# Optimization experiments

Hardware: AMD Instinct MI355X
Metric: run time of the kernel (lower is better)

## Reference

```python
import jax, jax.numpy as jnp
import numpy as np

B, S, HID = 2, 2048, 2048
H, KV, D = 16, 4, 128
EPS = 1e-6
ROPE_THETA = 1000000.0


def _rope_tables():
    inv_freq = 1.0 / (ROPE_THETA ** (jnp.arange(0, D, 2, dtype=jnp.float32) / D))  # [D/2]
    pos = jnp.arange(S, dtype=jnp.float32)
    freqs = pos[:, None] * inv_freq[None, :]            # [S, D/2]
    emb = jnp.concatenate([freqs, freqs], axis=-1)      # [S, D]
    cos = jnp.broadcast_to(jnp.cos(emb)[None], (B, S, D))
    sin = jnp.broadcast_to(jnp.sin(emb)[None], (B, S, D))
    return cos, sin


def setup_inputs() -> dict:
    key = jax.random.key(0)
    ks = jax.random.split(key, 6)
    cos, sin = _rope_tables()
    return {
        "hidden_states": jax.random.normal(ks[0], (B, S, HID), dtype=jnp.float32),
        "cos": cos,
        "sin": sin,
        "Wq": jax.random.normal(ks[1], (2 * H * D, HID), dtype=jnp.float32) * 0.02,
        "Wk": jax.random.normal(ks[2], (KV * D, HID), dtype=jnp.float32) * 0.02,
        "Wv": jax.random.normal(ks[3], (KV * D, HID), dtype=jnp.float32) * 0.02,
        "Wo": jax.random.normal(ks[4], (HID, H * D), dtype=jnp.float32) * 0.02,
        "q_norm_w": jnp.zeros((D,), dtype=jnp.float32),
        "k_norm_w": jnp.zeros((D,), dtype=jnp.float32),
    }


def _rms_norm(x, w):
    # (1+weight) parameterization, computed in fp32 as in the torch module
    xf = x.astype(jnp.float32)
    inv = jax.lax.rsqrt(jnp.mean(xf * xf, axis=-1, keepdims=True) + EPS)
    return (xf * inv * (1.0 + w.astype(jnp.float32))).astype(x.dtype)


def _rotate_half(x):
    h = x.shape[-1] // 2
    return jnp.concatenate([-x[..., h:], x[..., :h]], axis=-1)


def reference(hidden_states, cos, sin, Wq, Wk, Wv, Wo, q_norm_w, k_norm_w):
    b, s, _ = hidden_states.shape
    # Q projection yields interleaved (query, gate) per head: [B,S,H,2D]
    qg = jnp.einsum('bsh,oh->bso', hidden_states, Wq).reshape(b, s, H, 2 * D)
    q = qg[..., :D]                                   # [B,S,H,D]
    gate = qg[..., D:].reshape(b, s, H * D)           # [B,S,H*D]

    q = _rms_norm(q, q_norm_w).transpose(0, 2, 1, 3)                              # [B,H,S,D]
    k = _rms_norm(jnp.einsum('bsh,oh->bso', hidden_states, Wk).reshape(b, s, KV, D),
                  k_norm_w).transpose(0, 2, 1, 3)                                 # [B,KV,S,D]
    v = jnp.einsum('bsh,oh->bso', hidden_states, Wv).reshape(b, s, KV, D).transpose(0, 2, 1, 3)

    # RoPE (HF convention: cos/sin [B,S,D] broadcast over heads)
    c = cos[:, None, :, :]
    si = sin[:, None, :, :]
    q = q * c + _rotate_half(q) * si
    k = k * c + _rotate_half(k) * si

    # GQA repeat_kv: each kv head repeated n_rep times contiguously
    n_rep = H // KV
    k = jnp.repeat(k, n_rep, axis=1)   # [B,H,S,D]
    v = jnp.repeat(v, n_rep, axis=1)

    scale = D ** -0.5
    scores = jnp.einsum('bhqd,bhkd->bhqk', q, k) * scale                         # [B,H,S,S]
    causal = jnp.tril(jnp.ones((s, s), dtype=bool))
    scores = jnp.where(causal[None, None], scores, jnp.finfo(scores.dtype).min)
    probs = jax.nn.softmax(scores, axis=-1)
    attn = jnp.einsum('bhqk,bhkd->bhqd', probs, v)                               # [B,H,S,D]

    attn = attn.transpose(0, 2, 1, 3).reshape(b, s, H * D)
    attn = attn * jax.nn.sigmoid(gate)
    return jnp.einsum('bsh,oh->bso', attn, Wo)
```

## Files before the change

### kernel.cpp

```cpp
#include <hip/hip_runtime.h>
#include <stdint.h>


using bf16 = unsigned short;
typedef __attribute__((ext_vector_type(8)))  short bf16x8;
typedef __attribute__((ext_vector_type(4)))  float f32x4;
typedef __attribute__((ext_vector_type(16))) float f32x16;

__device__ __forceinline__ unsigned short f2bf(float x) {
  unsigned int u = __float_as_uint(x);
  unsigned int r = u + 0x7fffu + ((u >> 16) & 1u);
  return (unsigned short)(r >> 16);
}

__device__ __forceinline__ unsigned int pk2(float a, float b) {
  return (unsigned int)f2bf(a) | ((unsigned int)f2bf(b) << 16);
}

__device__ __forceinline__ void async_copy16(const void* g, void* l) {
  __builtin_amdgcn_global_load_lds(
      (const __attribute__((address_space(1))) void*)g,
      (__attribute__((address_space(3))) void*)l, 16, 0, 0);
}

__global__ void f2b_kernel(const float* __restrict__ in, bf16* __restrict__ out) {
  int i = (blockIdx.x * 256 + threadIdx.x) * 4;
  float4 v = *(const float4*)(in + i);
  ushort4 o;
  o.x = f2bf(v.x); o.y = f2bf(v.y); o.z = f2bf(v.z); o.w = f2bf(v.w);
  *(ushort4*)(out + i) = o;
}

__global__ __launch_bounds__(256) void gemm_bt(const bf16* __restrict__ A,
                                               const bf16* __restrict__ B,
                                               float* __restrict__ C,
                                               int M, int N, int K) {
  __shared__ __align__(16) bf16 As[128 * 32];
  __shared__ __align__(16) bf16 Bs[128 * 32];
  const int tid = threadIdx.x;
  const int w = tid >> 6, lane = tid & 63;
  const int wr = w >> 1, wc = w & 1;
  const int li = lane & 15, hi = lane >> 4;

  const int nbx = gridDim.x, nwg = nbx * gridDim.y;
  const int orig = blockIdx.y * nbx + blockIdx.x;
  const int tileid = (orig & 7) * (nwg >> 3) + (orig >> 3);
  const int bm = (tileid / nbx) * 128, bn = (tileid % nbx) * 128;

  f32x4 acc[4][4];
#pragma unroll
  for (int m = 0; m < 4; m++)
#pragma unroll
    for (int n = 0; n < 4; n++) acc[m][n] = (f32x4){0.f, 0.f, 0.f, 0.f};

  const int c0 = tid, c1 = tid + 256;
  const bf16* Ab = A + (long long)bm * K;
  const bf16* Bb = B + (long long)bn * K;

  for (int k0 = 0; k0 < K; k0 += 32) {
    async_copy16(Ab + (c0 >> 2) * K + k0 + (c0 & 3) * 8, (char*)As + c0 * 16);
    async_copy16(Ab + (c1 >> 2) * K + k0 + (c1 & 3) * 8, (char*)As + c1 * 16);
    async_copy16(Bb + (c0 >> 2) * K + k0 + (c0 & 3) * 8, (char*)Bs + c0 * 16);
    async_copy16(Bb + (c1 >> 2) * K + k0 + (c1 & 3) * 8, (char*)Bs + c1 * 16);
    __syncthreads();

    bf16x8 af[4], bfv[4];
#pragma unroll
    for (int m = 0; m < 4; m++)
      af[m] = *(const bf16x8*)(As + (wr * 64 + m * 16 + li) * 32 + hi * 8);
#pragma unroll
    for (int n = 0; n < 4; n++)
      bfv[n] = *(const bf16x8*)(Bs + (wc * 64 + n * 16 + li) * 32 + hi * 8);
#pragma unroll
    for (int m = 0; m < 4; m++)
#pragma unroll
      for (int n = 0; n < 4; n++)
        acc[m][n] = __builtin_amdgcn_mfma_f32_16x16x32_bf16(af[m], bfv[n],
                                                            acc[m][n], 0, 0, 0);
    __syncthreads();
  }

#pragma unroll
  for (int m = 0; m < 4; m++)
#pragma unroll
    for (int n = 0; n < 4; n++) {
      int row = bm + wr * 64 + m * 16 + hi * 4;
      int col = bn + wc * 64 + n * 16 + li;
#pragma unroll
      for (int r = 0; r < 4; r++) C[(long long)(row + r) * N + col] = acc[m][n][r];
    }
}

__global__ __launch_bounds__(256) void pack_qk(
    const float* __restrict__ qg_raw, const float* __restrict__ kv_raw,
    const float* __restrict__ cosb, const float* __restrict__ sinb,
    const float* __restrict__ qnw, const float* __restrict__ knw,
    bf16* __restrict__ q_pack, bf16* __restrict__ k_pack) {
  int rowid = blockIdx.x * 4 + (threadIdx.x >> 6);
  int lane = threadIdx.x & 63;
  int token = rowid / 20, r = rowid % 20;
  int b = token >> 11, s = token & 2047;
  const float* src; const float* wn; bf16* dst; float scale;
  if (r < 16) {
    src = qg_raw + (long long)token * 4096 + r * 256;
    wn = qnw;
    dst = q_pack + ((long long)(b * 16 + r) * 2048 + s) * 128;
    scale = 0.08838834764831845f;
  } else {
    int kv = r - 16;
    src = kv_raw + (long long)token * 1024 + kv * 128;
    wn = knw;
    dst = k_pack + ((long long)(b * 4 + kv) * 2048 + s) * 128;
    scale = 1.0f;
  }
  float x0 = src[lane], x1 = src[lane + 64];
  float ss = x0 * x0 + x1 * x1;
#pragma unroll
  for (int off = 32; off > 0; off >>= 1) ss += __shfl_xor(ss, off);
  float inv = rsqrtf(ss * (1.0f / 128.0f) + 1e-6f);
  float n0 = x0 * inv * (1.f + wn[lane]);
  float n1 = x1 * inv * (1.f + wn[lane + 64]);
  const float* cp = cosb + (long long)(b * 2048 + s) * 128;
  const float* sp = sinb + (long long)(b * 2048 + s) * 128;
  dst[lane]      = f2bf((n0 * cp[lane]      - n1 * sp[lane])      * scale);
  dst[lane + 64] = f2bf((n1 * cp[lane + 64] + n0 * sp[lane + 64]) * scale);
}

__global__ __launch_bounds__(256) void transpose_v(const float* __restrict__ kv_raw,
                                                   bf16* __restrict__ vt) {
  __shared__ float tile[32][33];
  int b = blockIdx.z;
  int c0 = blockIdx.x * 32;
  int s0 = blockIdx.y * 32;
  int tx = threadIdx.x & 31, ty = threadIdx.x >> 5;
#pragma unroll
  for (int i = 0; i < 32; i += 8)
    tile[ty + i][tx] = kv_raw[(long long)(b * 2048 + s0 + ty + i) * 1024 + 512 + c0 + tx];
  __syncthreads();
#pragma unroll
  for (int i = 0; i < 32; i += 8)
    vt[(long long)(b * 512 + c0 + ty + i) * 2048 + s0 + tx] = f2bf(tile[tx][ty + i]);
}

__global__ __launch_bounds__(256) void attn_kernel(
    const bf16* __restrict__ qp, const bf16* __restrict__ kp,
    const bf16* __restrict__ vt, const float* __restrict__ qg_raw,
    bf16* __restrict__ attn_g) {
  const int w = threadIdx.x >> 6, lane = threadIdx.x & 63;
  const int l31 = lane & 31, hi2 = lane >> 5;
  const int bh = blockIdx.y, b = bh >> 4, h = bh & 15, kv = h >> 2;
  const int qtile = (gridDim.x - 1) - blockIdx.x;
  const int q0w = qtile * 128 + w * 32;
  const int q = q0w + l31;

  const bf16* qb = qp + ((long long)(b * 16 + h) * 2048 + q0w) * 128;
  const bf16* kb = kp + (long long)(b * 4 + kv) * 2048 * 128;
  const bf16* vb = vt + (long long)(b * 4 + kv) * 128 * 2048;

  bf16x8 qf[8];
#pragma unroll
  for (int d = 0; d < 8; d++)
    qf[d] = *(const bf16x8*)(qb + l31 * 128 + d * 16 + hi2 * 8);

  f32x16 O[4];
#pragma unroll
  for (int ct = 0; ct < 4; ct++)
#pragma unroll
    for (int i = 0; i < 16; i++) O[ct][i] = 0.f;

  float mval = -1e30f, lsum = 0.f;
  const int ktmax = q0w >> 5;

  bf16x8 kf[8];
#pragma unroll
  for (int d = 0; d < 8; d++)
    kf[d] = *(const bf16x8*)(kb + l31 * 128 + d * 16 + hi2 * 8);

  for (int kt = 0; kt <= ktmax; kt++) {
    const int k0 = kt * 32;

    f32x16 s;
#pragma unroll
    for (int i = 0; i < 16; i++) s[i] = 0.f;
#pragma unroll
    for (int d = 0; d < 8; d++)
      s = __builtin_amdgcn_mfma_f32_32x32x16_bf16(kf[d], qf[d], s, 0, 0, 0);

    const int k0n = (kt < ktmax) ? (k0 + 32) : k0;
#pragma unroll
    for (int d = 0; d < 8; d++)
      kf[d] = *(const bf16x8*)(kb + (k0n + l31) * 128 + d * 16 + hi2 * 8);

    bf16x8 vf[8];
#pragma unroll
    for (int ct = 0; ct < 4; ct++)
#pragma unroll
      for (int kc = 0; kc < 2; kc++)
        vf[ct * 2 + kc] =
            *(const bf16x8*)(vb + (ct * 32 + l31) * 2048 + k0 + kc * 16 + hi2 * 8);

    if (k0 + 31 > q0w) {
#pragma unroll
      for (int r = 0; r < 16; r++) {
        int kk = k0 + (r & 3) + 8 * (r >> 2) + 4 * hi2;
        if (kk > q) s[r] = -1e30f;
      }
    }

    float pm = s[0];
#pragma unroll
    for (int r = 1; r < 16; r++) pm = fmaxf(pm, s[r]);
    pm = fmaxf(pm, __shfl_xor(pm, 32));

    int keep = __all(pm <= mval + 8.0f);
    float mn = mval, alpha = 1.f;
    if (!keep) {
      mn = fmaxf(mval, pm);
      alpha = __expf(mval - mn);
      mval = mn;
    }
    float sum = 0.f;
#pragma unroll
    for (int r = 0; r < 16; r++) { s[r] = __expf(s[r] - mn); sum += s[r]; }
    sum += __shfl_xor(sum, 32);
    if (keep) {
      lsum += sum;
    } else {
      lsum = lsum * alpha + sum;
#pragma unroll
      for (int ct = 0; ct < 4; ct++)
#pragma unroll
        for (int i = 0; i < 16; i++) O[ct][i] *= alpha;
    }

    bf16x8 pf[2];
#pragma unroll
    for (int kc = 0; kc < 2; kc++) {
      unsigned int wA = pk2(s[8 * kc + 0], s[8 * kc + 1]);
      unsigned int wB = pk2(s[8 * kc + 2], s[8 * kc + 3]);
      unsigned int wC = pk2(s[8 * kc + 4], s[8 * kc + 5]);
      unsigned int wD = pk2(s[8 * kc + 6], s[8 * kc + 7]);
      unsigned int xA = (unsigned int)__shfl_xor((int)wA, 32);
      unsigned int xB = (unsigned int)__shfl_xor((int)wB, 32);
      unsigned int xC = (unsigned int)__shfl_xor((int)wC, 32);
      unsigned int xD = (unsigned int)__shfl_xor((int)wD, 32);
      union { unsigned int u[4]; bf16x8 v; } pu;
      pu.u[0] = hi2 ? xC : wA;
      pu.u[1] = hi2 ? xD : wB;
      pu.u[2] = hi2 ? wC : xA;
      pu.u[3] = hi2 ? wD : xB;
      pf[kc] = pu.v;
    }

#pragma unroll
    for (int ct = 0; ct < 4; ct++) {
      O[ct] = __builtin_amdgcn_mfma_f32_32x32x16_bf16(vf[ct * 2 + 0], pf[0], O[ct], 0, 0, 0);
      O[ct] = __builtin_amdgcn_mfma_f32_32x32x16_bf16(vf[ct * 2 + 1], pf[1], O[ct], 0, 0, 0);
    }
  }

  const float linv = 1.f / lsum;
  const long long tok = (long long)(b * 2048 + q);
#pragma unroll
  for (int ct = 0; ct < 4; ct++)
#pragma unroll
    for (int r = 0; r < 16; r++) {
      int c = ct * 32 + (r & 3) + 8 * (r >> 2) + 4 * hi2;
      float g = qg_raw[tok * 4096 + h * 256 + 128 + c];
      float val = O[ct][r] * linv * (1.f / (1.f + __expf(-g)));
      attn_g[tok * 2048 + h * 128 + c] = f2bf(val);
    }
}

extern "C" void kernel_launch(void* const* d_in, const int* in_sizes, int n_in,
                              void* d_out, int out_size, void* d_ws, size_t ws_size,
                              hipStream_t stream) {
  const float* hs   = (const float*)d_in[0];
  const float* cosb = (const float*)d_in[1];
  const float* sinb = (const float*)d_in[2];
  const float* Wq   = (const float*)d_in[3];
  const float* Wk   = (const float*)d_in[4];
  const float* Wv   = (const float*)d_in[5];
  const float* Wo   = (const float*)d_in[6];
  const float* qnw  = (const float*)d_in[7];
  const float* knw  = (const float*)d_in[8];
  float* out = (float*)d_out;

  const size_t WS_NEEDED = 130023424ull;
  if (ws_size < WS_NEEDED) return;

  char* p = (char*)d_ws;
  bf16*  hs_bf  = (bf16*)p;  p += 4096ull * 2048 * 2;
  bf16*  wq_bf  = (bf16*)p;  p += 4096ull * 2048 * 2;
  bf16*  wkv_bf = (bf16*)p;  p += 1024ull * 2048 * 2;
  bf16*  wo_bf  = (bf16*)p;  p += 2048ull * 2048 * 2;
  float* qg_raw = (float*)p; p += 4096ull * 4096 * 4;
  float* kv_raw = (float*)p; p += 4096ull * 1024 * 4;
  bf16* q_pack = (bf16*)hs_bf;
  bf16* k_pack = (bf16*)wq_bf;
  bf16* vt     = (bf16*)((char*)wq_bf + 2ull * 4 * 2048 * 128 * 2);
  bf16* attn_g = (bf16*)kv_raw;

  f2b_kernel<<<8192, 256, 0, stream>>>(hs, hs_bf);
  f2b_kernel<<<8192, 256, 0, stream>>>(Wq, wq_bf);
  f2b_kernel<<<1024, 256, 0, stream>>>(Wk, wkv_bf);
  f2b_kernel<<<1024, 256, 0, stream>>>(Wv, wkv_bf + 512 * 2048);
  f2b_kernel<<<4096, 256, 0, stream>>>(Wo, wo_bf);

  gemm_bt<<<dim3(32, 32), 256, 0, stream>>>(hs_bf, wq_bf, qg_raw, 4096, 4096, 2048);
  gemm_bt<<<dim3(8, 32), 256, 0, stream>>>(hs_bf, wkv_bf, kv_raw, 4096, 1024, 2048);

  pack_qk<<<20480, 256, 0, stream>>>(qg_raw, kv_raw, cosb, sinb, qnw, knw, q_pack, k_pack);
  transpose_v<<<dim3(16, 64, 2), 256, 0, stream>>>(kv_raw, vt);

  attn_kernel<<<dim3(16, 32), 256, 0, stream>>>(q_pack, k_pack, vt, qg_raw, attn_g);

  gemm_bt<<<dim3(16, 32), 256, 0, stream>>>(attn_g, wo_bf, out, 4096, 2048, 2048);
}
```

Measured before the change: 612.4 us.

## Stage K/V tiles in LDS with double-buffered async copies shared across waves

The attention kernel now loads each 32-key K tile and V tile once per block into swizzled LDS buffers using async global-to-LDS copies. It double-buffers them so the next tile is fetched while the current one is computed, and all four waves share the tile instead of each reading it from global memory. The V transpose kernel writes a tile-blocked layout so each key tile is one contiguous 8 KB chunk. The cost is a block-wide barrier every iteration and a block-uniform loop bound, so lower waves run extra fully masked tiles.

Result: faster. 557.4 us (-9.0%).

```diff
diff --git a/kernel.cpp b/kernel.cpp
--- a/kernel.cpp
+++ b/kernel.cpp
@@ -137,15 +137,21 @@
   for (int i = 0; i < 32; i += 8)
     tile[ty + i][tx] = kv_raw[(long long)(b * 2048 + s0 + ty + i) * 1024 + 512 + c0 + tx];
   __syncthreads();
-#pragma unroll
-  for (int i = 0; i < 32; i += 8)
-    vt[(long long)(b * 512 + c0 + ty + i) * 2048 + s0 + tx] = f2bf(tile[tx][ty + i]);
+  int kt = s0 >> 5;
+#pragma unroll
+  for (int i = 0; i < 32; i += 8) {
+    int cg = c0 + ty + i;
+    int kvh = cg >> 7, c = cg & 127;
+    vt[((long long)(b * 4 + kvh) * 64 + kt) * 4096 + c * 32 + tx] = f2bf(tile[tx][ty + i]);
+  }
 }
 
 __global__ __launch_bounds__(256) void attn_kernel(
     const bf16* __restrict__ qp, const bf16* __restrict__ kp,
     const bf16* __restrict__ vt, const float* __restrict__ qg_raw,
     bf16* __restrict__ attn_g) {
+  __shared__ __align__(16) char Ks[2][8192];
+  __shared__ __align__(16) char Vs[2][8192];
   const int w = threadIdx.x >> 6, lane = threadIdx.x & 63;
   const int l31 = lane & 31, hi2 = lane >> 5;
   const int bh = blockIdx.y, b = bh >> 4, h = bh & 15, kv = h >> 2;
@@ -154,8 +160,19 @@
   const int q = q0w + l31;
 
   const bf16* qb = qp + ((long long)(b * 16 + h) * 2048 + q0w) * 128;
-  const bf16* kb = kp + (long long)(b * 4 + kv) * 2048 * 128;
-  const bf16* vb = vt + (long long)(b * 4 + kv) * 128 * 2048;
+  const char* kbb = (const char*)(kp + (long long)(b * 4 + kv) * 2048 * 128);
+  const char* vbb = (const char*)(vt + (long long)(b * 4 + kv) * 64 * 4096);
+
+  int ksrco[2], vsrco[2], dsto[2];
+#pragma unroll
+  for (int i = 0; i < 2; i++) {
+    int p = (w * 2 + i) * 64 + lane;
+    int rk = p >> 4, gk = p & 15;
+    ksrco[i] = rk * 256 + ((gk ^ (rk & 15)) << 4);
+    int rv = p >> 2, gv = p & 3;
+    vsrco[i] = rv * 64 + ((gv ^ ((rv >> 1) & 3)) << 4);
+    dsto[i] = p << 4;
+  }
 
   bf16x8 qf[8];
 #pragma unroll
@@ -169,15 +186,40 @@
     for (int i = 0; i < 16; i++) O[ct][i] = 0.f;
 
   float mval = -1e30f, lsum = 0.f;
-  const int ktmax = q0w >> 5;
-
-  bf16x8 kf[8];
-#pragma unroll
-  for (int d = 0; d < 8; d++)
-    kf[d] = *(const bf16x8*)(kb + l31 * 128 + d * 16 + hi2 * 8);
-
-  for (int kt = 0; kt <= ktmax; kt++) {
+  const int ktmaxb = qtile * 4 + 3;
+
+#pragma unroll
+  for (int i = 0; i < 2; i++) {
+    async_copy16(kbb + ksrco[i], &Ks[0][dsto[i]]);
+    async_copy16(vbb + vsrco[i], &Vs[0][dsto[i]]);
+  }
+  __syncthreads();
+
+  for (int kt = 0; kt <= ktmaxb; kt++) {
+    const int bi = kt & 1;
     const int k0 = kt * 32;
+
+    if (kt < ktmaxb) {
+      const char* ksrc = kbb + (long long)(kt + 1) * 8192;
+      const char* vsrc = vbb + (long long)(kt + 1) * 8192;
+#pragma unroll
+      for (int i = 0; i < 2; i++) {
+        async_copy16(ksrc + ksrco[i], &Ks[bi ^ 1][dsto[i]]);
+        async_copy16(vsrc + vsrco[i], &Vs[bi ^ 1][dsto[i]]);
+      }
+    }
+
+    bf16x8 kf[8];
+#pragma unroll
+    for (int d = 0; d < 8; d++)
+      kf[d] = *(const bf16x8*)&Ks[bi][l31 * 256 + (((d * 2 + hi2) ^ (l31 & 15)) << 4)];
+    bf16x8 vf[8];
+#pragma unroll
+    for (int ct = 0; ct < 4; ct++)
+#pragma unroll
+      for (int kc = 0; kc < 2; kc++)
+        vf[ct * 2 + kc] = *(const bf16x8*)
+            &Vs[bi][(ct * 32 + l31) * 64 + (((kc * 2 + hi2) ^ ((l31 >> 1) & 3)) << 4)];
 
     f32x16 s;
 #pragma unroll
@@ -185,19 +227,6 @@
 #pragma unroll
     for (int d = 0; d < 8; d++)
       s = __builtin_amdgcn_mfma_f32_32x32x16_bf16(kf[d], qf[d], s, 0, 0, 0);
-
-    const int k0n = (kt < ktmax) ? (k0 + 32) : k0;
-#pragma unroll
-    for (int d = 0; d < 8; d++)
-      kf[d] = *(const bf16x8*)(kb + (k0n + l31) * 128 + d * 16 + hi2 * 8);
-
-    bf16x8 vf[8];
-#pragma unroll
-    for (int ct = 0; ct < 4; ct++)
-#pragma unroll
-      for (int kc = 0; kc < 2; kc++)
-        vf[ct * 2 + kc] =
-            *(const bf16x8*)(vb + (ct * 32 + l31) * 2048 + k0 + kc * 16 + hi2 * 8);
 
     if (k0 + 31 > q0w) {
 #pragma unroll
@@ -257,6 +286,8 @@
       O[ct] = __builtin_amdgcn_mfma_f32_32x32x16_bf16(vf[ct * 2 + 0], pf[0], O[ct], 0, 0, 0);
       O[ct] = __builtin_amdgcn_mfma_f32_32x32x16_bf16(vf[ct * 2 + 1], pf[1], O[ct], 0, 0, 0);
     }
+
+    __syncthreads();
   }
 
   const float linv = 1.f / lsum;
```
